# Kernel optimization log

Hardware: AMD Instinct MI355X
Metric: run time of the kernel (lower is better)

## Reference

```python
import jax, jax.numpy as jnp
import numpy as np

H = 450       # hidden_size (JTNN decoder default)
V = 800       # junction-tree vocab size
N_NODES = 4000
N_MESS = 6000
K = 6         # max neighbors (padded)
B = 256       # number of trees / roots
DH = 450      # netD hidden size
DEPTH = 15


def setup_inputs() -> dict:
    key = jax.random.key(0)
    ks = jax.random.split(key, 16)

    def w(k, shape, fan_in):
        return jax.random.normal(k, shape, dtype=jnp.float32) / np.float32(np.sqrt(fan_in))

    inp = {}
    inp["fnode"] = jax.random.randint(ks[0], (N_NODES,), 0, V)
    inp["fmess"] = jax.random.randint(ks[1], (N_MESS,), 0, N_NODES)
    inp["node_graph"] = jax.random.randint(ks[2], (N_NODES, K), 0, N_MESS)
    inp["mess_graph"] = jax.random.randint(ks[3], (N_MESS, K), 0, N_MESS)
    inp["root_idx"] = jax.random.randint(ks[4], (B,), 0, N_NODES)
    # Generator (JTNN decoder GRU) params; weights stored torch-style [out, in]
    inp["emb"] = w(ks[5], (V, H), H)
    inp["W_z_w"] = w(ks[6], (H, 2 * H), 2 * H)
    inp["W_z_b"] = jnp.zeros((H,), jnp.float32)
    inp["W_r_w"] = w(ks[7], (H, H), H)          # bias=False in JTNN
    inp["U_r_w"] = w(ks[8], (H, H), H)
    inp["U_r_b"] = jnp.zeros((H,), jnp.float32)
    inp["W_h_w"] = w(ks[9], (H, 2 * H), 2 * H)
    inp["W_h_b"] = jnp.zeros((H,), jnp.float32)
    # netD: Linear(2H,DH) -> LeakyReLU(0.1) -> Linear(DH,DH) -> LeakyReLU(0.1) -> Linear(DH,1)
    inp["D1_w"] = w(ks[10], (DH, 2 * H), 2 * H)
    inp["D1_b"] = jnp.zeros((DH,), jnp.float32)
    inp["D2_w"] = w(ks[11], (DH, DH), DH)
    inp["D2_b"] = jnp.zeros((DH,), jnp.float32)
    inp["D3_w"] = w(ks[12], (1, DH), DH)
    inp["D3_b"] = jnp.zeros((1,), jnp.float32)
    inp["depth"] = DEPTH
    return inp


def _generator(fnode, fmess, node_graph, mess_graph, root_idx,
               emb, W_z_w, W_z_b, W_r_w, U_r_w, U_r_b, W_h_w, W_h_b, depth):
    fnode_e = emb[fnode]                      # [N, H] embedding lookup
    x = fnode_e[fmess]                        # [M, H] source-node features per message
    M = fmess.shape[0]
    mask = jnp.ones((M, 1), jnp.float32).at[0].set(0.0)   # message 0 is padding
    h0 = jnp.zeros((M, emb.shape[1]), jnp.float32)

    def step(h, _):
        h_nei = h[mess_graph]                 # [M, K, H] gather of incoming messages
        sum_h = h_nei.sum(axis=1)             # [M, H]
        z = jax.nn.sigmoid(jnp.concatenate([x, sum_h], axis=-1) @ W_z_w.T + W_z_b)
        r = jax.nn.sigmoid((x @ W_r_w.T)[:, None, :] + h_nei @ U_r_w.T + U_r_b)
        sum_gh = (r * h_nei).sum(axis=1)
        pre_h = jnp.tanh(jnp.concatenate([x, sum_gh], axis=-1) @ W_h_w.T + W_h_b)
        h_new = ((1.0 - z) * sum_h + z * pre_h) * mask
        return h_new, None

    h, _ = jax.lax.scan(step, h0, None, length=depth)
    mess_nei = h[node_graph].sum(axis=1)      # [N, H]
    node_vecs = jnp.concatenate([fnode_e, mess_nei], axis=-1)   # [N, 2H]
    return node_vecs[root_idx]                # [B, 2H]


def reference(fnode, fmess, node_graph, mess_graph, root_idx,
              emb, W_z_w, W_z_b, W_r_w, U_r_w, U_r_b, W_h_w, W_h_b,
              D1_w, D1_b, D2_w, D2_b, D3_w, D3_b, depth):
    root_vecs = _generator(fnode, fmess, node_graph, mess_graph, root_idx,
                           emb, W_z_w, W_z_b, W_r_w, U_r_w, U_r_b, W_h_w, W_h_b, depth)
    h1 = jax.nn.leaky_relu(root_vecs @ D1_w.T + D1_b, 0.1)
    h2 = jax.nn.leaky_relu(h1 @ D2_w.T + D2_b, 0.1)
    score = (h2 @ D3_w.T + D3_b).squeeze(-1)  # [B] discriminator scores
    return score
```

## Files before the change

kernel.cpp:

```cpp
#include <hip/hip_runtime.h>
#include <stdint.h>
#include <stddef.h>

#define NMSG   6000
#define NNODE  4000
#define HDIM   450
#define KNEI   6
#define NB     256
#define KP     480
#define MP     6016
#define NPAD   512
#define DEPTH_C 15
#define GX     96
#define GROWS  6016

typedef unsigned short u16;
typedef __attribute__((ext_vector_type(8))) short short8;
typedef __attribute__((ext_vector_type(4))) float f32x4;

__device__ __forceinline__ float b2f(u16 h) { return __uint_as_float(((unsigned)h) << 16); }
__device__ __forceinline__ u16 f2b(float f) {
    unsigned u = __float_as_uint(f);
    return (u16)((u + 0x7FFFu + ((u >> 16) & 1u)) >> 16);
}
__device__ __forceinline__ void fsplit(float f, u16& hi, u16& lo) {
    u16 h = f2b(f);
    hi = h;
    lo = f2b(f - b2f(h));
}
__device__ __forceinline__ float gload(const void* p, size_t i, int isb) {
    return isb ? b2f(((const u16*)p)[i]) : ((const float*)p)[i];
}

__device__ __forceinline__ void gload_lds16(const void* g, void* l) {
    __builtin_amdgcn_global_load_lds((const __attribute__((address_space(1))) unsigned int*)g,
                                     (__attribute__((address_space(3))) unsigned int*)l,
                                     16, 0, 0);
}

__device__ __forceinline__ int xcd_row(int b) {
    if (b >= 5632) return b;
    int c = b & 7, u = b >> 3;
    return 512 * (u >> 6) + 64 * c + (u & 63);
}

__global__ void zero_kernel(uint4* p, size_t n16) {
    size_t i = (size_t)blockIdx.x * blockDim.x + threadIdx.x;
    size_t stride = (size_t)gridDim.x * blockDim.x;
    uint4 z = make_uint4(0, 0, 0, 0);
    for (; i < n16; i += stride) p[i] = z;
}

__global__ void detect_kernel(const void* __restrict__ emb, int* __restrict__ flagp) {
    __shared__ int cnt;
    if (threadIdx.x == 0) cnt = 0;
    __syncthreads();
    const u16* p = (const u16*)emb;
    int c = 0;
#pragma unroll
    for (int j = 0; j < 8; ++j) {
        u16 u = p[2 * (threadIdx.x * 8 + j)];
        int e = (u >> 7) & 0xFF;
        if (u == 0 || u == 0x8000u || (e >= 64 && e <= 127)) c++;
    }
    atomicAdd(&cnt, c);
    __syncthreads();
    if (threadIdx.x == 0) *flagp = (cnt > 1300) ? 1 : 0;
}

__global__ void prep_kernel(const void* __restrict__ Wz, const void* __restrict__ Wr,
                            const void* __restrict__ Ur, const void* __restrict__ Wh,
                            const void* __restrict__ D1w, const void* __restrict__ D2w,
                            u16* __restrict__ wb, float* __restrict__ d1t, float* __restrict__ d2t,
                            const int* __restrict__ flagp) {
    const int isb = *flagp;
    int job = blockIdx.y;
    int idx = blockIdx.x * 256 + threadIdx.x;
    if (job < 6) {
        if (idx >= NPAD * KP) return;
        int n = idx / KP, k = idx % KP;
        u16 vh = 0, vl = 0;
        if (n < HDIM && k < HDIM) {
            float f;
            switch (job) {
                case 0: f = gload(Wz, (size_t)n * 900 + k, isb); break;
                case 1: f = gload(Wz, (size_t)n * 900 + 450 + k, isb); break;
                case 2: f = gload(Wr, (size_t)n * 450 + k, isb); break;
                case 3: f = gload(Ur, (size_t)n * 450 + k, isb); break;
                case 4: f = gload(Wh, (size_t)n * 900 + k, isb); break;
                default: f = gload(Wh, (size_t)n * 900 + 450 + k, isb); break;
            }
            fsplit(f, vh, vl);
        }
        wb[(size_t)job * NPAD * KP + idx] = vh;
        wb[(size_t)(job + 6) * NPAD * KP + idx] = vl;
    } else if (job == 6) {
        if (idx >= 900 * 450) return;
        int i = idx / 450, j = idx % 450;
        d1t[i * 450 + j] = gload(D1w, (size_t)j * 900 + i, isb);
    } else {
        if (idx >= 450 * 450) return;
        int i = idx / 450, j = idx % 450;
        d2t[i * 450 + j] = gload(D2w, (size_t)j * 450 + i, isb);
    }
}

__global__ void xgather_kernel(const int* __restrict__ fnode, const int* __restrict__ fmess,
                               const void* __restrict__ emb, u16* __restrict__ xh,
                               u16* __restrict__ xl, const int* __restrict__ flagp) {
    const int isb = *flagp;
    int m = xcd_row(blockIdx.x);
    int c = threadIdx.x * 2;
    if (m >= NMSG || c >= HDIM) return;
    int src = fnode[fmess[m]];
    float f0, f1;
    if (isb) {
        unsigned u = *(const unsigned*)((const u16*)emb + (size_t)src * HDIM + c);
        f0 = b2f((u16)u); f1 = b2f((u16)(u >> 16));
    } else {
        float2 v = *(const float2*)((const float*)emb + (size_t)src * HDIM + c);
        f0 = v.x; f1 = v.y;
    }
    u16 h0, l0, h1, l1;
    fsplit(f0, h0, l0);
    fsplit(f1, h1, l1);
    *(unsigned*)(xh + (size_t)m * KP + c) = (unsigned)h0 | ((unsigned)h1 << 16);
    *(unsigned*)(xl + (size_t)m * KP + c) = (unsigned)l0 | ((unsigned)l1 << 16);
}

__global__ void init_h_kernel(const u16* __restrict__ xwzb, const u16* __restrict__ xwhb,
                              u16* __restrict__ hbh, u16* __restrict__ hbl) {
    int m = xcd_row(blockIdx.x);
    int c = threadIdx.x * 2;
    if (m >= NMSG || c >= HDIM) return;
    size_t o = (size_t)m * HDIM + c;
    unsigned zv = *(const unsigned*)(xwzb + o);
    unsigned hv = *(const unsigned*)(xwhb + o);
    u16 oh[2], ol[2];
#pragma unroll
    for (int q = 0; q < 2; ++q) {
        float aP = b2f((u16)(q ? (hv >> 16) : hv));
        float e = __expf(2.f * aP);
        float pre = 1.f - 2.f / (e + 1.f);
        float aZ = b2f((u16)(q ? (zv >> 16) : zv));
        float z = 1.f / (1.f + __expf(-aZ));
        float hn = z * pre;
        if (m == 0) hn = 0.f;
        fsplit(hn, oh[q], ol[q]);
    }
    size_t ok = (size_t)m * KP + c;
    *(unsigned*)(hbh + ok) = (unsigned)oh[0] | ((unsigned)oh[1] << 16);
    *(unsigned*)(hbl + ok) = (unsigned)ol[0] | ((unsigned)ol[1] << 16);
}

__global__ void gather_kernel(const u16* __restrict__ hh, const u16* __restrict__ hl,
                              const u16* __restrict__ uhb, const u16* __restrict__ xwrb,
                              const void* __restrict__ urb, const int* __restrict__ mg,
                              u16* __restrict__ shfh, u16* __restrict__ shfl,
                              u16* __restrict__ sgh, const int* __restrict__ flagp) {
    const int isb = *flagp;
    int m = xcd_row(blockIdx.x);
    int c = threadIdx.x * 2;
    if (m >= NMSG || c >= HDIM) return;
    const int* ng = mg + m * KNEI;
    size_t o = (size_t)m * HDIM + c;
    unsigned xv = *(const unsigned*)(xwrb + o);
    float xr0 = b2f((u16)xv), xr1 = b2f((u16)(xv >> 16));
    float b0 = gload(urb, c, isb);
    float b1 = gload(urb, c + 1, isb);
    float s0 = 0.f, s1 = 0.f;
    float g0 = 0.f, g1 = 0.f;
#pragma unroll
    for (int k = 0; k < KNEI; ++k) {
        int nm = ng[k];
        size_t oh = (size_t)nm * KP + c;
        unsigned vh = *(const unsigned*)(hh + oh);
        unsigned vl = *(const unsigned*)(hl + oh);
        float hv0 = b2f((u16)vh) + b2f((u16)vl);
        float hv1 = b2f((u16)(vh >> 16)) + b2f((u16)(vl >> 16));
        s0 += hv0; s1 += hv1;
        unsigned uv = *(const unsigned*)(uhb + (size_t)nm * HDIM + c);
        float a0 = xr0 + b2f((u16)uv) + b0;
        float a1 = xr1 + b2f((u16)(uv >> 16)) + b1;
        g0 += hv0 / (1.f + __expf(-a0));
        g1 += hv1 / (1.f + __expf(-a1));
    }
    size_t ok = (size_t)m * KP + c;
    u16 sh0, sl0, sh1, sl1;
    fsplit(s0, sh0, sl0);
    fsplit(s1, sh1, sl1);
    *(unsigned*)(shfh + ok) = (unsigned)sh0 | ((unsigned)sh1 << 16);
    *(unsigned*)(shfl + ok) = (unsigned)sl0 | ((unsigned)sl1 << 16);
    *(unsigned*)(sgh + ok) = (unsigned)f2b(g0) | ((unsigned)f2b(g1) << 16);
}

struct GemmDesc {
    const u16* Ah;
    const u16* Al;
    const u16* Bh;
    const u16* Bl;
    const void* bias;
    u16* outb;
    int ostride;
    int ooff;
};

__global__ __launch_bounds__(256, 5) void gemm_kernel(GemmDesc d0, GemmDesc d1, GemmDesc d2,
                                                      const int* __restrict__ flagp) {
    if (blockIdx.x >= 94) return;
    GemmDesc d = (blockIdx.z == 0) ? d0 : ((blockIdx.z == 1) ? d1 : d2);
    const int isb = *flagp;
    __shared__ __align__(16) u16 lds[2][4][64 * 32];
    const int tid = threadIdx.x;
    const int wave = tid >> 6, lane = tid & 63;
    const int m0 = blockIdx.x * 64;
    const int n0 = blockIdx.y * 64;
    const int wm = wave & 1, wn = wave >> 1;
    const int lhi = lane >> 4, llo = lane & 15;
    const int cx = (lhi ^ ((llo >> 1) & 3)) * 8;

    f32x4 acc[2][2];
#pragma unroll
    for (int i = 0; i < 2; i++)
#pragma unroll
        for (int j = 0; j < 2; j++) acc[i][j] = (f32x4){0.f, 0.f, 0.f, 0.f};

    const int rl = lane >> 2, cl = lane & 3;
    const int csw = cl ^ ((rl >> 1) & 3);
    const u16* ssrc = (wave == 0) ? d.Ah : (wave == 1) ? d.Al : (wave == 2) ? d.Bh : d.Bl;
    const int srb = (wave < 2) ? m0 : n0;
    const u16* gbase = ssrc + (size_t)(srb + rl) * KP + csw * 8;

    auto stage = [&](int b, int kt) {
#pragma unroll
        for (int q = 0; q < 4; ++q)
            gload_lds16(gbase + (size_t)q * 16 * KP + kt * 32, &lds[b][wave][q * 512]);
    };

    auto compute = [&](const u16* buf) {
        short8 afh[2], afl[2], bfh[2], bfl[2];
#pragma unroll
        for (int i = 0; i < 2; i++) {
            const int off = (wm * 32 + i * 16 + llo) * 32 + cx;
            afh[i] = *(const short8*)(buf + off);
            afl[i] = *(const short8*)(buf + 2048 + off);
        }
#pragma unroll
        for (int j = 0; j < 2; j++) {
            const int off = (wn * 32 + j * 16 + llo) * 32 + cx;
            bfh[j] = *(const short8*)(buf + 4096 + off);
            bfl[j] = *(const short8*)(buf + 6144 + off);
        }
#pragma unroll
        for (int i = 0; i < 2; i++)
#pragma unroll
            for (int j = 0; j < 2; j++) {
                acc[i][j] = __builtin_amdgcn_mfma_f32_16x16x32_bf16(afh[i], bfl[j], acc[i][j], 0, 0, 0);
                acc[i][j] = __builtin_amdgcn_mfma_f32_16x16x32_bf16(afl[i], bfh[j], acc[i][j], 0, 0, 0);
                acc[i][j] = __builtin_amdgcn_mfma_f32_16x16x32_bf16(afh[i], bfh[j], acc[i][j], 0, 0, 0);
            }
    };

    stage(0, 0);
    __syncthreads();

    int p = 0;
#pragma unroll 1
    for (int kt = 1; kt < KP / 32; ++kt) {
        stage(p ^ 1, kt);
        compute(&lds[p][0][0]);
        __syncthreads();
        p ^= 1;
    }
    compute(&lds[p][0][0]);

#pragma unroll
    for (int i = 0; i < 2; i++) {
#pragma unroll
        for (int j = 0; j < 2; j++) {
            int n = n0 + wn * 32 + j * 16 + llo;
            int mb = m0 + wm * 32 + i * 16 + lhi * 4;
            if (n >= HDIM) continue;
#pragma unroll
            for (int r = 0; r < 4; r++) {
                int m = mb + r;
                if (m >= NMSG) continue;
                size_t o = (size_t)m * HDIM + n;
                float v = acc[i][j][r];
                if (d.bias) v += gload(d.bias, n, isb);
                d.outb[o * d.ostride + d.ooff] = f2b(v);
            }
        }
    }
}

__global__ __launch_bounds__(256, 3) void gemm3d_kernel(
        const u16* __restrict__ sgh, const u16* __restrict__ shfh, const u16* __restrict__ shfl,
        const u16* __restrict__ bWhhh, const u16* __restrict__ bWhhl,
        const u16* __restrict__ bWzhh, const u16* __restrict__ bWzhl,
        const u16* __restrict__ xwhb, const u16* __restrict__ xwzb,
        u16* __restrict__ hbh, u16* __restrict__ hbl) {
    if (blockIdx.x >= 94) return;
    __shared__ __align__(16) u16 lds[2][12288];
    const int tid = threadIdx.x;
    const int wave = tid >> 6, lane = tid & 63;
    const int m0 = blockIdx.x * 64;
    const int n0 = blockIdx.y * 64;
    const int wm = wave & 1, wn = wave >> 1;
    const int lhi = lane >> 4, llo = lane & 15;
    const int cx = (lhi ^ ((llo >> 1) & 3)) * 8;

    const int rl = lane >> 2, cl = lane & 3;
    const int csw = cl ^ ((rl >> 1) & 3);
    const int row = wave * 16 + rl;
    const size_t aoff = (size_t)(m0 + row) * KP + csw * 8;
    const size_t boff = (size_t)(n0 + row) * KP + csw * 8;
    const int ldst = wave * 512;

    f32x4 accP[2][2], accZ[2][2];
#pragma unroll
    for (int i = 0; i < 2; i++)
#pragma unroll
        for (int j = 0; j < 2; j++) {
            accP[i][j] = (f32x4){0.f, 0.f, 0.f, 0.f};
            accZ[i][j] = (f32x4){0.f, 0.f, 0.f, 0.f};
        }

    auto stage = [&](int b, int kt) {
        const size_t ko = (size_t)kt * 32;
        gload_lds16(sgh   + aoff + ko, &lds[b][0     + ldst]);
        gload_lds16(shfh  + aoff + ko, &lds[b][2048  + ldst]);
        gload_lds16(bWhhh + boff + ko, &lds[b][4096  + ldst]);
        gload_lds16(bWhhl + boff + ko, &lds[b][6144  + ldst]);
        gload_lds16(bWzhh + boff + ko, &lds[b][8192  + ldst]);
        gload_lds16(bWzhl + boff + ko, &lds[b][10240 + ldst]);
    };

    auto compute = [&](const u16* buf) {
        short8 as_[2], ah[2], bwh[2], bwl[2], bzh[2], bzl[2];
#pragma unroll
        for (int i = 0; i < 2; i++) {
            const int off = (wm * 32 + i * 16 + llo) * 32 + cx;
            as_[i] = *(const short8*)(buf + off);
            ah[i]  = *(const short8*)(buf + 2048 + off);
        }
#pragma unroll
        for (int j = 0; j < 2; j++) {
            const int off = (wn * 32 + j * 16 + llo) * 32 + cx;
            bwh[j] = *(const short8*)(buf + 4096 + off);
            bwl[j] = *(const short8*)(buf + 6144 + off);
            bzh[j] = *(const short8*)(buf + 8192 + off);
            bzl[j] = *(const short8*)(buf + 10240 + off);
        }
#pragma unroll
        for (int i = 0; i < 2; i++)
#pragma unroll
            for (int j = 0; j < 2; j++) {
                accP[i][j] = __builtin_amdgcn_mfma_f32_16x16x32_bf16(as_[i], bwl[j], accP[i][j], 0, 0, 0);
                accP[i][j] = __builtin_amdgcn_mfma_f32_16x16x32_bf16(as_[i], bwh[j], accP[i][j], 0, 0, 0);
                accZ[i][j] = __builtin_amdgcn_mfma_f32_16x16x32_bf16(ah[i], bzl[j], accZ[i][j], 0, 0, 0);
                accZ[i][j] = __builtin_amdgcn_mfma_f32_16x16x32_bf16(ah[i], bzh[j], accZ[i][j], 0, 0, 0);
            }
    };

    stage(0, 0);
    __syncthreads();
    int p = 0;
#pragma unroll 1
    for (int kt = 1; kt < KP / 32; ++kt) {
        stage(p ^ 1, kt);
        compute(&lds[p][0]);
        __syncthreads();
        p ^= 1;
    }
    compute(&lds[p][0]);

#pragma unroll
    for (int i = 0; i < 2; i++) {
#pragma unroll
        for (int j = 0; j < 2; j++) {
            int n = n0 + wn * 32 + j * 16 + llo;
            int mb = m0 + wm * 32 + i * 16 + lhi * 4;
            if (n >= HDIM) continue;
#pragma unroll
            for (int r = 0; r < 4; r++) {
                int m = mb + r;
                if (m >= NMSG) continue;
                size_t o = (size_t)m * HDIM + n;
                size_t ob = (size_t)m * KP + n;
                float aP = accP[i][j][r] + b2f(xwhb[o]);
                float e = __expf(2.f * aP);
                float pre = 1.f - 2.f / (e + 1.f);
                float aZ = accZ[i][j][r] + b2f(xwzb[o]);
                float z = 1.f / (1.f + __expf(-aZ));
                float shv = b2f(shfh[ob]) + b2f(shfl[ob]);
                float hn = (1.f - z) * shv + z * pre;
                if (m == 0) hn = 0.f;
                fsplit(hn, hbh[ob], hbl[ob]);
            }
        }
    }
}

__global__ void root_kernel(const int* __restrict__ root_idx, const int* __restrict__ fnode,
                            const int* __restrict__ node_graph, const void* __restrict__ emb,
                            const u16* __restrict__ hh, const u16* __restrict__ hl,
                            float* __restrict__ rv, const int* __restrict__ flagp) {
    const int isb = *flagp;
    int b = blockIdx.x, c = threadIdx.x;
    if (c >= HDIM) return;
    int node = root_idx[b];
    rv[(size_t)b * 900 + c] = gload(emb, (size_t)fnode[node] * HDIM + c, isb);
    const int* ng = node_graph + node * KNEI;
    float s = 0.f;
#pragma unroll
    for (int k = 0; k < KNEI; ++k) {
        size_t o = (size_t)ng[k] * KP + c;
        s += b2f(hh[o]) + b2f(hl[o]);
    }
    rv[(size_t)b * 900 + 450 + c] = s;
}

__global__ void mlp_kernel(const float* __restrict__ rv, const float* __restrict__ d1t,
                           const void* __restrict__ D1b, const float* __restrict__ d2t,
                           const void* __restrict__ D2b, const void* __restrict__ D3w,
                           const void* __restrict__ D3b, void* __restrict__ out,
                           const int* __restrict__ flagp) {
    const int isb = *flagp;
    __shared__ float xs[900];
    __shared__ float h1s[450];
    __shared__ float red[8];
    int b = blockIdx.x, t = threadIdx.x;
    for (int i = t; i < 900; i += 512) xs[i] = rv[(size_t)b * 900 + i];
    __syncthreads();
    float a1 = 0.f;
    if (t < 450) {
        for (int i = 0; i < 900; ++i) a1 = fmaf(xs[i], d1t[i * 450 + t], a1);
        a1 += gload(D1b, t, isb);
        a1 = a1 > 0.f ? a1 : 0.1f * a1;
        h1s[t] = a1;
    }
    __syncthreads();
    float a2 = 0.f;
    if (t < 450) {
        for (int i = 0; i < 450; ++i) a2 = fmaf(h1s[i], d2t[i * 450 + t], a2);
        a2 += gload(D2b, t, isb);
        a2 = a2 > 0.f ? a2 : 0.1f * a2;
        a2 *= gload(D3w, t, isb);
    }
#pragma unroll
    for (int o = 32; o > 0; o >>= 1) a2 += __shfl_down(a2, o, 64);
    if ((t & 63) == 0) red[t >> 6] = a2;
    __syncthreads();
    if (t == 0) {
        float s = gload(D3b, 0, isb);
#pragma unroll
        for (int w = 0; w < 8; ++w) s += red[w];
        if (isb) ((u16*)out)[b] = f2b(s);
        else     ((float*)out)[b] = s;
    }
}

extern "C" void kernel_launch(void* const* d_in, const int* in_sizes, int n_in,
                              void* d_out, int out_size, void* d_ws, size_t ws_size,
                              hipStream_t stream) {
    const int* fnode      = (const int*)d_in[0];
    const int* fmess      = (const int*)d_in[1];
    const int* node_graph = (const int*)d_in[2];
    const int* mess_graph = (const int*)d_in[3];
    const int* root_idx   = (const int*)d_in[4];
    const void* emb = d_in[5];
    const void* Wz  = d_in[6];
    const void* Wzb = d_in[7];
    const void* Wr  = d_in[8];
    const void* Ur  = d_in[9];
    const void* Urb = d_in[10];
    const void* Wh  = d_in[11];
    const void* Whb = d_in[12];
    const void* D1w = d_in[13];
    const void* D1b = d_in[14];
    const void* D2w = d_in[15];
    const void* D2b = d_in[16];
    const void* D3w = d_in[17];
    const void* D3b = d_in[18];

    char* ws = (char*)d_ws;
    size_t off = 0;
    auto alloc = [&](size_t bytes) {
        char* p = ws + off;
        off += (bytes + 255) & ~(size_t)255;
        return p;
    };
    const size_t SZ_B16 = (size_t)MP * KP * 2;
    const size_t SZ_H16 = (size_t)NMSG * HDIM * 2;
    const size_t SZ_W   = (size_t)NPAD * KP * 2;

    int* flagp = (int*)alloc(256);
    u16* xbh   = (u16*)alloc(SZ_B16);
    u16* xbl   = (u16*)alloc(SZ_B16);
    u16* hbh   = (u16*)alloc(SZ_B16);
    u16* hbl   = (u16*)alloc(SZ_B16);
    u16* sgbh  = (u16*)alloc(SZ_B16);
    u16* shfh  = (u16*)alloc(SZ_B16);
    u16* shfl  = (u16*)alloc(SZ_B16);
    size_t zero_bytes = off;

    u16* uhb   = (u16*)alloc(SZ_H16);
    u16* xwzb  = (u16*)alloc(SZ_H16);
    u16* xwrb  = (u16*)alloc(SZ_H16);
    u16* xwhb  = (u16*)alloc(SZ_H16);
    u16* wb    = (u16*)alloc(12 * SZ_W);
    float* d1t = (float*)alloc(900 * 450 * 4);
    float* d2t = (float*)alloc(450 * 450 * 4);
    float* rv  = (float*)alloc((size_t)NB * 900 * 4);
    (void)ws_size; (void)in_sizes; (void)n_in; (void)out_size;

    const size_t WP = (size_t)NPAD * KP;
    u16* bWzxh = wb + 0 * WP;  u16* bWzxl = wb + 6 * WP;
    u16* bWzhh = wb + 1 * WP;  u16* bWzhl = wb + 7 * WP;
    u16* bWrh  = wb + 2 * WP;  u16* bWrl  = wb + 8 * WP;
    u16* bUrh  = wb + 3 * WP;  u16* bUrl  = wb + 9 * WP;
    u16* bWhxh = wb + 4 * WP;  u16* bWhxl = wb + 10 * WP;
    u16* bWhhh = wb + 5 * WP;  u16* bWhhl = wb + 11 * WP;

    zero_kernel<<<2048, 256, 0, stream>>>((uint4*)ws, zero_bytes / 16);
    detect_kernel<<<1, 256, 0, stream>>>(emb, flagp);
    prep_kernel<<<dim3(1583, 8), 256, 0, stream>>>(Wz, Wr, Ur, Wh, D1w, D2w,
                                                   wb, d1t, d2t, flagp);
    xgather_kernel<<<GROWS, 256, 0, stream>>>(fnode, fmess, emb, xbh, xbl, flagp);

    GemmDesc g0 = { xbh, xbl, bWzxh, bWzxl, Wzb, xwzb, 1, 0 };
    GemmDesc g1 = { xbh, xbl, bWrh,  bWrl,  nullptr, xwrb, 1, 0 };
    GemmDesc g2 = { xbh, xbl, bWhxh, bWhxl, Whb, xwhb, 1, 0 };
    gemm_kernel<<<dim3(GX, 8, 3), 256, 0, stream>>>(g0, g1, g2, flagp);

    init_h_kernel<<<GROWS, 256, 0, stream>>>(xwzb, xwhb, hbh, hbl);

    GemmDesc du = { hbh, hbl, bUrh, bUrl, nullptr, uhb, 1, 0 };
    for (int t = 1; t < DEPTH_C; ++t) {
        gemm_kernel<<<dim3(GX, 8, 1), 256, 0, stream>>>(du, du, du, flagp);
        gather_kernel<<<GROWS, 256, 0, stream>>>(hbh, hbl, uhb, xwrb, Urb,
                                                 mess_graph, shfh, shfl, sgbh, flagp);
        gemm3d_kernel<<<dim3(GX, 8), 256, 0, stream>>>(sgbh, shfh, shfl, bWhhh, bWhhl,
                                                       bWzhh, bWzhl, xwhb, xwzb,
                                                       hbh, hbl);
    }

    root_kernel<<<NB, 512, 0, stream>>>(root_idx, fnode, node_graph, emb, hbh, hbl, rv, flagp);
    mlp_kernel<<<NB, 512, 0, stream>>>(rv, d1t, D1b, d2t, D2b, D3w, D3b, d_out, flagp);
}
```

Before: 1.126 ms.

## Load GEMM weight tiles directly into registers instead of staging through LDS

In both GEMM kernels, only the activation (A) tiles are still staged through shared memory. Each wave now reads its weight (B) fragments straight from global memory into registers, with a one-step register prefetch. This shrinks LDS per block and removes the LDS writes and reads for B. In exchange it uses more registers (the launch-bounds occupancy hint drops from 5 to 4 for gemm_kernel). It also fetches B redundantly across the waves that share the same column half, relying on cache hits.

```diff
diff --git a/kernel.cpp b/kernel.cpp
--- a/kernel.cpp
+++ b/kernel.cpp
@@ -205,12 +205,12 @@
     int ooff;
 };
 
-__global__ __launch_bounds__(256, 5) void gemm_kernel(GemmDesc d0, GemmDesc d1, GemmDesc d2,
+__global__ __launch_bounds__(256, 4) void gemm_kernel(GemmDesc d0, GemmDesc d1, GemmDesc d2,
                                                       const int* __restrict__ flagp) {
     if (blockIdx.x >= 94) return;
     GemmDesc d = (blockIdx.z == 0) ? d0 : ((blockIdx.z == 1) ? d1 : d2);
     const int isb = *flagp;
-    __shared__ __align__(16) u16 lds[2][4][64 * 32];
+    __shared__ __align__(16) u16 lds[2][4096];
     const int tid = threadIdx.x;
     const int wave = tid >> 6, lane = tid & 63;
     const int m0 = blockIdx.x * 64;
@@ -227,29 +227,32 @@
 
     const int rl = lane >> 2, cl = lane & 3;
     const int csw = cl ^ ((rl >> 1) & 3);
-    const u16* ssrc = (wave == 0) ? d.Ah : (wave == 1) ? d.Al : (wave == 2) ? d.Bh : d.Bl;
-    const int srb = (wave < 2) ? m0 : n0;
-    const u16* gbase = ssrc + (size_t)(srb + rl) * KP + csw * 8;
+    const int pl = wave >> 1, half = wave & 1;
+    const u16* asrc = (pl ? d.Al : d.Ah) + (size_t)(m0 + half * 32 + rl) * KP + csw * 8;
+    const int abase = pl * 2048 + half * 1024;
 
     auto stage = [&](int b, int kt) {
-#pragma unroll
-        for (int q = 0; q < 4; ++q)
-            gload_lds16(gbase + (size_t)q * 16 * KP + kt * 32, &lds[b][wave][q * 512]);
-    };
-
-    auto compute = [&](const u16* buf) {
-        short8 afh[2], afl[2], bfh[2], bfl[2];
+        gload_lds16(asrc + kt * 32, &lds[b][abase]);
+        gload_lds16(asrc + (size_t)16 * KP + kt * 32, &lds[b][abase + 512]);
+    };
+
+    const u16* Bh = d.Bh + (size_t)(n0 + wn * 32 + llo) * KP + lhi * 8;
+    const u16* Bl = d.Bl + (size_t)(n0 + wn * 32 + llo) * KP + lhi * 8;
+    auto loadB = [&](int kt, short8 bh[2], short8 bl[2]) {
+#pragma unroll
+        for (int j = 0; j < 2; j++) {
+            bh[j] = *(const short8*)(Bh + (size_t)j * 16 * KP + kt * 32);
+            bl[j] = *(const short8*)(Bl + (size_t)j * 16 * KP + kt * 32);
+        }
+    };
+
+    auto compute = [&](const u16* buf, const short8 bfh[2], const short8 bfl[2]) {
+        short8 afh[2], afl[2];
 #pragma unroll
         for (int i = 0; i < 2; i++) {
             const int off = (wm * 32 + i * 16 + llo) * 32 + cx;
             afh[i] = *(const short8*)(buf + off);
             afl[i] = *(const short8*)(buf + 2048 + off);
-        }
-#pragma unroll
-        for (int j = 0; j < 2; j++) {
-            const int off = (wn * 32 + j * 16 + llo) * 32 + cx;
-            bfh[j] = *(const short8*)(buf + 4096 + off);
-            bfl[j] = *(const short8*)(buf + 6144 + off);
         }
 #pragma unroll
         for (int i = 0; i < 2; i++)
@@ -261,18 +264,23 @@
             }
     };
 
+    short8 cbh[2], cbl[2], nbh[2], nbl[2];
     stage(0, 0);
+    loadB(0, cbh, cbl);
     __syncthreads();
 
     int p = 0;
 #pragma unroll 1
     for (int kt = 1; kt < KP / 32; ++kt) {
         stage(p ^ 1, kt);
-        compute(&lds[p][0][0]);
+        loadB(kt, nbh, nbl);
+        compute(&lds[p][0], cbh, cbl);
         __syncthreads();
+#pragma unroll
+        for (int j = 0; j < 2; j++) { cbh[j] = nbh[j]; cbl[j] = nbl[j]; }
         p ^= 1;
     }
-    compute(&lds[p][0][0]);
+    compute(&lds[p][0], cbh, cbl);
 
 #pragma unroll
     for (int i = 0; i < 2; i++) {
@@ -301,7 +309,7 @@
         const u16* __restrict__ xwhb, const u16* __restrict__ xwzb,
         u16* __restrict__ hbh, u16* __restrict__ hbl) {
     if (blockIdx.x >= 94) return;
-    __shared__ __align__(16) u16 lds[2][12288];
+    __shared__ __align__(16) u16 lds[2][4096];
     const int tid = threadIdx.x;
     const int wave = tid >> 6, lane = tid & 63;
     const int m0 = blockIdx.x * 64;
@@ -312,10 +320,30 @@
 
     const int rl = lane >> 2, cl = lane & 3;
     const int csw = cl ^ ((rl >> 1) & 3);
-    const int row = wave * 16 + rl;
-    const size_t aoff = (size_t)(m0 + row) * KP + csw * 8;
-    const size_t boff = (size_t)(n0 + row) * KP + csw * 8;
-    const int ldst = wave * 512;
+    const int pl = wave >> 1, half = wave & 1;
+    const u16* asrc = (pl ? shfh : sgh) + (size_t)(m0 + half * 32 + rl) * KP + csw * 8;
+    const int abase = pl * 2048 + half * 1024;
+
+    auto stage = [&](int b, int kt) {
+        gload_lds16(asrc + kt * 32, &lds[b][abase]);
+        gload_lds16(asrc + (size_t)16 * KP + kt * 32, &lds[b][abase + 512]);
+    };
+
+    const size_t wboff = (size_t)(n0 + wn * 32 + llo) * KP + lhi * 8;
+    const u16* Wh_h = bWhhh + wboff;
+    const u16* Wh_l = bWhhl + wboff;
+    const u16* Wz_h = bWzhh + wboff;
+    const u16* Wz_l = bWzhl + wboff;
+    auto loadB = [&](int kt, short8 bwh[2], short8 bwl[2], short8 bzh[2], short8 bzl[2]) {
+#pragma unroll
+        for (int j = 0; j < 2; j++) {
+            const size_t o = (size_t)j * 16 * KP + kt * 32;
+            bwh[j] = *(const short8*)(Wh_h + o);
+            bwl[j] = *(const short8*)(Wh_l + o);
+            bzh[j] = *(const short8*)(Wz_h + o);
+            bzl[j] = *(const short8*)(Wz_l + o);
+        }
+    };
 
     f32x4 accP[2][2], accZ[2][2];
 #pragma unroll
@@ -326,31 +354,14 @@
             accZ[i][j] = (f32x4){0.f, 0.f, 0.f, 0.f};
         }
 
-    auto stage = [&](int b, int kt) {
-        const size_t ko = (size_t)kt * 32;
-        gload_lds16(sgh   + aoff + ko, &lds[b][0     + ldst]);
-        gload_lds16(shfh  + aoff + ko, &lds[b][2048  + ldst]);
-        gload_lds16(bWhhh + boff + ko, &lds[b][4096  + ldst]);
-        gload_lds16(bWhhl + boff + ko, &lds[b][6144  + ldst]);
-        gload_lds16(bWzhh + boff + ko, &lds[b][8192  + ldst]);
-        gload_lds16(bWzhl + boff + ko, &lds[b][10240 + ldst]);
-    };
-
-    auto compute = [&](const u16* buf) {
-        short8 as_[2], ah[2], bwh[2], bwl[2], bzh[2], bzl[2];
+    auto compute = [&](const u16* buf, const short8 bwh[2], const short8 bwl[2],
+                       const short8 bzh[2], const short8 bzl[2]) {
+        short8 as_[2], ah[2];
 #pragma unroll
         for (int i = 0; i < 2; i++) {
             const int off = (wm * 32 + i * 16 + llo) * 32 + cx;
             as_[i] = *(const short8*)(buf + off);
             ah[i]  = *(const short8*)(buf + 2048 + off);
-        }
-#pragma unroll
-        for (int j = 0; j < 2; j++) {
-            const int off = (wn * 32 + j * 16 + llo) * 32 + cx;
-            bwh[j] = *(const short8*)(buf + 4096 + off);
-            bwl[j] = *(const short8*)(buf + 6144 + off);
-            bzh[j] = *(const short8*)(buf + 8192 + off);
-            bzl[j] = *(const short8*)(buf + 10240 + off);
         }
 #pragma unroll
         for (int i = 0; i < 2; i++)
@@ -363,17 +374,24 @@
             }
     };
 
+    short8 cwh[2], cwl[2], czh[2], czl[2], nwh[2], nwl[2], nzh[2], nzl[2];
     stage(0, 0);
+    loadB(0, cwh, cwl, czh, czl);
     __syncthreads();
     int p = 0;
 #pragma unroll 1
     for (int kt = 1; kt < KP / 32; ++kt) {
         stage(p ^ 1, kt);
-        compute(&lds[p][0]);
+        loadB(kt, nwh, nwl, nzh, nzl);
+        compute(&lds[p][0], cwh, cwl, czh, czl);
         __syncthreads();
+#pragma unroll
+        for (int j = 0; j < 2; j++) {
+            cwh[j] = nwh[j]; cwl[j] = nwl[j]; czh[j] = nzh[j]; czl[j] = nzl[j];
+        }
         p ^= 1;
     }
-    compute(&lds[p][0]);
+    compute(&lds[p][0], cwh, cwl, czh, czl);
 
 #pragma unroll
     for (int i = 0; i < 2; i++) {
```

After: 1.340 ms. 18.9% more time.
